# Kernel optimization log

Measured on AMD Instinct MI355X. Metric: run time of the kernel, lower is better.

## Reference

```python
import jax, jax.numpy as jnp
import numpy as np

D_MODEL = 256
NHEAD = 8
NLAYERS = 4
DFF = 1024
PATCH = 8
INPUT = 32
C = 2
DATA_DIM = C * PATCH * PATCH  # 128
P = (INPUT // PATCH) ** 2     # 16
NEG = -1.0e6                  # _neg_large_for_dtype(float32)
EPS = 1e-5


def _ln(x, w, b):
    m = x.mean(-1, keepdims=True)
    v = ((x - m) ** 2).mean(-1, keepdims=True)
    return (x - m) / jnp.sqrt(v + EPS) * w + b


def _forward(img_baseline, acq_dts_float, nan_token, pad_embed, emb_w, emb_b, spatial_pos,
             t_w1, t_b1, t_w2, t_b2, t_w3, t_b3,
             in_proj_w, in_proj_b, out_proj_w, out_proj_b,
             lin1_w, lin1_b, lin2_w, lin2_b, norm1_w, norm1_b, norm2_w, norm2_b,
             mean_w1, mean_b1, mean_w2, mean_b2, lv_w1, lv_b1, lv_w2, lv_b2):
    B, T, Cc, Hh, Ww = img_baseline.shape
    p = PATCH
    gh, gw = Hh // p, Ww // p
    L = T * P
    frame_pad = jnp.all(img_baseline == -9999.0, axis=(2, 3, 4))  # (B,T)
    nan_pix = jnp.isnan(img_baseline)
    token = jnp.clip(nan_token, -10.0, 10.0).reshape(1, 1, Cc, 1, 1)
    x = jnp.clip(jnp.where(nan_pix, token, img_baseline), -10.0, 10.0)

    def patchify(a):  # b t c (h ph)(w pw) -> b t (h w) (c ph pw)
        return a.reshape(B, T, Cc, gh, p, gw, p).transpose(0, 1, 3, 5, 2, 4, 6).reshape(B, T, P, Cc * p * p)

    xp = patchify(x)
    seq_nan = patchify(nan_pix).all(-1).reshape(B, L)
    seq_pad = jnp.broadcast_to(frame_pad[:, :, None], (B, T, P)).reshape(B, L)

    # temporal MLP embedding
    t_in = jnp.where(jnp.isnan(acq_dts_float), 0.0, acq_dts_float)[..., None]  # (B,T,1)
    h = jax.nn.relu(t_in @ t_w1.T + t_b1)
    h = jax.nn.relu(h @ t_w2.T + t_b2)
    temb = h @ t_w3.T + t_b3  # (B,T,D)

    z = xp @ emb_w.T + emb_b + spatial_pos + temb[:, :, None, :]  # (B,T,P,D)
    z = z.reshape(B, L, D_MODEL)
    z = jnp.where(seq_pad[..., None], pad_embed, z)  # masked_scatter of pad_embed

    # additive attention mask: rows with NaN/pad patches are fully masked except diagonal
    masked_rows = seq_nan | seq_pad
    mask = jnp.broadcast_to(jnp.where(masked_rows[:, :, None], NEG, 0.0), (B, L, L))
    eye = jnp.eye(L, dtype=bool)
    mask = jnp.where(eye[None, :, :] & masked_rows[:, :, None], 0.0, mask)
    # key_padding_mask merged additively on key columns
    mask = mask + jnp.where(seq_pad[:, None, :], NEG, 0.0)
    mask = mask[:, None, :, :]  # (B,1,L,L), shared across heads

    dh = D_MODEL // NHEAD
    scale = 1.0 / np.sqrt(dh).astype(np.float32)
    for l in range(NLAYERS):
        qkv = z @ in_proj_w[l].T + in_proj_b[l]
        q, k, v = jnp.split(qkv, 3, axis=-1)
        q = q.reshape(B, L, NHEAD, dh).transpose(0, 2, 1, 3)
        k = k.reshape(B, L, NHEAD, dh).transpose(0, 2, 1, 3)
        v = v.reshape(B, L, NHEAD, dh).transpose(0, 2, 1, 3)
        scores = jnp.einsum('bhqd,bhkd->bhqk', q, k) * scale + mask
        attn = jax.nn.softmax(scores, axis=-1)
        o = jnp.einsum('bhqk,bhkd->bhqd', attn, v).transpose(0, 2, 1, 3).reshape(B, L, D_MODEL)
        o = o @ out_proj_w[l].T + out_proj_b[l]
        z = _ln(z + o, norm1_w[l], norm1_b[l])
        ff = jax.nn.relu(z @ lin1_w[l].T + lin1_b[l]) @ lin2_w[l].T + lin2_b[l]
        z = _ln(z + ff, norm2_w[l], norm2_b[l])

    mean = jnp.clip(jax.nn.relu(z @ mean_w1.T + mean_b1) @ mean_w2.T + mean_b2, -10.0, 10.0)
    logvar = jnp.clip(jax.nn.relu(z @ lv_w1.T + lv_b1) @ lv_w2.T + lv_b2, -10.0, 5.0)

    def unpatch(a):  # b t (h w)(c ph pw) -> b t c (h ph)(w pw)
        return a.reshape(B, T, gh, gw, Cc, p, p).transpose(0, 1, 4, 2, 5, 3, 6).reshape(B, T, Cc, Hh, Ww)

    mean = unpatch(mean.reshape(B, T, P, DATA_DIM))
    logvar = unpatch(logvar.reshape(B, T, P, DATA_DIM))
    return mean[:, -1], logvar[:, -1]


def setup_inputs() -> dict:
    key = jax.random.key(0)
    ks = iter(jax.random.split(key, 48))

    def rn(shape, scale=0.02):
        return jax.random.normal(next(ks), shape, dtype=jnp.float32) * scale

    B, T = 4, 64
    z = lambda s: jnp.zeros(s, jnp.float32)
    return {
        'img_baseline': jax.random.normal(next(ks), (B, T, C, INPUT, INPUT), dtype=jnp.float32),
        'acq_dts_float': jax.random.uniform(next(ks), (B, T), dtype=jnp.float32) * 3000.0,
        'nan_token': rn((C,)),
        'pad_embed': rn((1, 1, D_MODEL)),
        'emb_w': rn((D_MODEL, DATA_DIM)),
        'emb_b': z((D_MODEL,)),
        'spatial_pos': rn((1, 1, P, D_MODEL)),
        't_w1': rn((64, 1)), 't_b1': z((64,)),
        't_w2': rn((128, 64)), 't_b2': z((128,)),
        't_w3': rn((D_MODEL, 128)), 't_b3': z((D_MODEL,)),
        'in_proj_w': rn((NLAYERS, 3 * D_MODEL, D_MODEL)),
        'in_proj_b': z((NLAYERS, 3 * D_MODEL)),
        'out_proj_w': rn((NLAYERS, D_MODEL, D_MODEL)),
        'out_proj_b': z((NLAYERS, D_MODEL)),
        'lin1_w': rn((NLAYERS, DFF, D_MODEL)), 'lin1_b': z((NLAYERS, DFF)),
        'lin2_w': rn((NLAYERS, D_MODEL, DFF)), 'lin2_b': z((NLAYERS, D_MODEL)),
        'norm1_w': jnp.ones((NLAYERS, D_MODEL), jnp.float32), 'norm1_b': z((NLAYERS, D_MODEL)),
        'norm2_w': jnp.ones((NLAYERS, D_MODEL), jnp.float32), 'norm2_b': z((NLAYERS, D_MODEL)),
        'mean_w1': rn((DFF, D_MODEL)), 'mean_b1': z((DFF,)),
        'mean_w2': rn((DATA_DIM, DFF)), 'mean_b2': z((DATA_DIM,)),
        'lv_w1': rn((DFF, D_MODEL)), 'lv_b1': z((DFF,)),
        'lv_w2': rn((DATA_DIM, DFF)), 'lv_b2': z((DATA_DIM,)),
    }


def reference(img_baseline, acq_dts_float, nan_token, pad_embed, emb_w, emb_b, spatial_pos,
              t_w1, t_b1, t_w2, t_b2, t_w3, t_b3,
              in_proj_w, in_proj_b, out_proj_w, out_proj_b,
              lin1_w, lin1_b, lin2_w, lin2_b, norm1_w, norm1_b, norm2_w, norm2_b,
              mean_w1, mean_b1, mean_w2, mean_b2, lv_w1, lv_b1, lv_w2, lv_b2):
    return _forward(img_baseline, acq_dts_float, nan_token, pad_embed, emb_w, emb_b, spatial_pos,
                    t_w1, t_b1, t_w2, t_b2, t_w3, t_b3,
                    in_proj_w, in_proj_b, out_proj_w, out_proj_b,
                    lin1_w, lin1_b, lin2_w, lin2_b, norm1_w, norm1_b, norm2_w, norm2_b,
                    mean_w1, mean_b1, mean_w2, mean_b2, lv_w1, lv_b1, lv_w2, lv_b2)
```

## Files before the change

### kernel.cpp

```cpp
#include <hip/hip_runtime.h>
#include <hip/hip_bf16.h>

#define D_MODEL 256
#define NHEAD 8
#define DH 32
#define NLAYERS 4
#define DFF 1024
#define CC 2
#define DATA_DIM 128
#define PP 16
#define TT 64
#define BB 4
#define LL 1024
#define NEGV -1000000.0f

typedef __bf16 bf16_t;
typedef __bf16 bf16x8 __attribute__((ext_vector_type(8)));
typedef __bf16 bf16x4 __attribute__((ext_vector_type(4)));
typedef float v4f __attribute__((ext_vector_type(4)));

__device__ __forceinline__ bool my_isnan(float v) {
    unsigned u = __float_as_uint(v);
    return (u & 0x7fffffffu) > 0x7f800000u;
}

__device__ __forceinline__ void gld16(bf16_t* l, const bf16_t* g) {
    __builtin_amdgcn_global_load_lds(
        (const __attribute__((address_space(1))) void*)g,
        (__attribute__((address_space(3))) void*)l, 16, 0, 0);
}

__global__ void f2b_all_kernel(const float* __restrict__ s0, bf16_t* __restrict__ d0, int n0,
                               const float* __restrict__ s1, bf16_t* __restrict__ d1, int n1,
                               const float* __restrict__ s2, bf16_t* __restrict__ d2, int n2,
                               const float* __restrict__ s3, bf16_t* __restrict__ d3, int n3,
                               const float* __restrict__ s4, bf16_t* __restrict__ d4, int n4,
                               const float* __restrict__ s5, bf16_t* __restrict__ d5, int n5,
                               const float* __restrict__ s6, bf16_t* __restrict__ d6, int n6,
                               const float* __restrict__ s7, bf16_t* __restrict__ d7, int n7,
                               const float* __restrict__ s8, bf16_t* __restrict__ d8, int n8) {
    int i = (blockIdx.x * 256 + threadIdx.x) * 4;
    const float* s;
    bf16_t* d;
    if (i < n0) { s = s0; d = d0; }
    else if ((i -= n0) < n1) { s = s1; d = d1; }
    else if ((i -= n1) < n2) { s = s2; d = d2; }
    else if ((i -= n2) < n3) { s = s3; d = d3; }
    else if ((i -= n3) < n4) { s = s4; d = d4; }
    else if ((i -= n4) < n5) { s = s5; d = d5; }
    else if ((i -= n5) < n6) { s = s6; d = d6; }
    else if ((i -= n6) < n7) { s = s7; d = d7; }
    else if ((i -= n7) < n8) { s = s8; d = d8; }
    else return;
    float4 v = *(const float4*)(s + i);
    bf16x4 o = {(bf16_t)v.x, (bf16_t)v.y, (bf16_t)v.z, (bf16_t)v.w};
    *(bf16x4*)(d + i) = o;
}

__global__ void prep_frame_kernel(const float* __restrict__ img,
                                  const float* __restrict__ acq,
                                  const float* __restrict__ t_w1, const float* __restrict__ t_b1,
                                  const float* __restrict__ t_w2, const float* __restrict__ t_b2,
                                  const float* __restrict__ t_w3, const float* __restrict__ t_b3,
                                  float* __restrict__ temb, int* __restrict__ framepad) {
    int f = blockIdx.x;
    int tid = threadIdx.x;
    __shared__ float h1[64];
    __shared__ float h2[128];
    __shared__ int sAll;
    if (tid == 0) sAll = 1;
    __syncthreads();
    const float* fr = img + (size_t)f * (CC * 32 * 32);
    bool allpad = true;
    #pragma unroll
    for (int i = 0; i < 8; ++i) {
        float v = fr[tid + i * 256];
        allpad = allpad && (v == -9999.0f);
    }
    if (!allpad) sAll = 0;
    __syncthreads();
    if (tid == 0) framepad[f] = sAll;

    float t_in = acq[f];
    if (my_isnan(t_in)) t_in = 0.0f;
    if (tid < 64) h1[tid] = fmaxf(t_w1[tid] * t_in + t_b1[tid], 0.0f);
    __syncthreads();
    if (tid < 128) {
        float a = t_b2[tid];
        #pragma unroll 8
        for (int j = 0; j < 64; ++j) a += t_w2[tid * 64 + j] * h1[j];
        h2[tid] = fmaxf(a, 0.0f);
    }
    __syncthreads();
    {
        float a = t_b3[tid];
        #pragma unroll 8
        for (int j = 0; j < 128; ++j) a += t_w3[tid * 128 + j] * h2[j];
        temb[(size_t)f * D_MODEL + tid] = a;
    }
}

__global__ __launch_bounds__(256) void patchify_kernel(
    const float* __restrict__ img, const float* __restrict__ nan_token,
    const int* __restrict__ framepad,
    bf16_t* __restrict__ xpb, int* __restrict__ masked_rows,
    float* __restrict__ kmaskf) {
    int tid = threadIdx.x;
    int token = blockIdx.x * 2 + (tid >> 7);
    int dd = tid & 127;
    int l = token & 1023, b = token >> 10;
    int t = l >> 4, p = l & 15;
    int c = dd >> 6, pr = (dd >> 3) & 7, pc = dd & 7;
    int hh = (p >> 2) * 8 + pr, ww = (p & 3) * 8 + pc;
    float v = img[(((size_t)(b * TT + t) * CC + c) * 32 + hh) * 32 + ww];
    bool nanp = my_isnan(v);
    if (nanp) v = fminf(fmaxf(nan_token[c], -10.0f), 10.0f);
    v = fminf(fmaxf(v, -10.0f), 10.0f);
    xpb[(size_t)token * DATA_DIM + dd] = (bf16_t)v;

    __shared__ int wAll[4];
    unsigned long long bal = __ballot(nanp);
    if ((tid & 63) == 0) wAll[tid >> 6] = (bal == 0xFFFFFFFFFFFFFFFFull) ? 1 : 0;
    __syncthreads();
    if (tid < 2) {
        int tk = blockIdx.x * 2 + tid;
        int allnan = wAll[tid * 2] & wAll[tid * 2 + 1];
        int fp = framepad[tk >> 4];
        masked_rows[tk] = allnan | fp;
        kmaskf[tk] = fp ? NEGV : 0.0f;
    }
}

__global__ __launch_bounds__(256) void embed_gemm(
    const bf16_t* __restrict__ X, const bf16_t* __restrict__ W,
    const float* __restrict__ emb_b, const float* __restrict__ spatial,
    const float* __restrict__ temb, const float* __restrict__ pad_embed,
    const int* __restrict__ framepad,
    float* __restrict__ z, bf16_t* __restrict__ zb) {
    __shared__ __align__(16) bf16_t Xs[128 * 32];
    __shared__ __align__(16) bf16_t Ws[64 * 32];
    int tid = threadIdx.x;
    int wave = tid >> 6, lane = tid & 63;
    int quad = lane >> 4, l16 = lane & 15;
    int m0 = blockIdx.y * 128, n0 = blockIdx.x * 64;
    const int K = DATA_DIM, N = D_MODEL;

    v4f acc[2][4];
    #pragma unroll
    for (int i = 0; i < 2; ++i)
        #pragma unroll
        for (int j = 0; j < 4; ++j) acc[i][j] = (v4f){0.f, 0.f, 0.f, 0.f};

    int sr = tid >> 2, ss = tid & 3;
    for (int k0 = 0; k0 < K; k0 += 32) {
        gld16(Xs + tid * 8, X + (size_t)(m0 + sr) * K + k0 + ss * 8);
        gld16(Xs + 2048 + tid * 8, X + (size_t)(m0 + 64 + sr) * K + k0 + ss * 8);
        gld16(Ws + tid * 8, W + (size_t)(n0 + sr) * K + k0 + ss * 8);
        __syncthreads();
        bf16x8 af0 = *(const bf16x8*)(Xs + (wave * 32 + l16) * 32 + quad * 8);
        bf16x8 af1 = *(const bf16x8*)(Xs + (wave * 32 + 16 + l16) * 32 + quad * 8);
        #pragma unroll
        for (int nt = 0; nt < 4; ++nt) {
            bf16x8 bfr = *(const bf16x8*)(Ws + (nt * 16 + l16) * 32 + quad * 8);
            acc[0][nt] = __builtin_amdgcn_mfma_f32_16x16x32_bf16(af0, bfr, acc[0][nt], 0, 0, 0);
            acc[1][nt] = __builtin_amdgcn_mfma_f32_16x16x32_bf16(af1, bfr, acc[1][nt], 0, 0, 0);
        }
        __syncthreads();
    }

    #pragma unroll
    for (int mt = 0; mt < 2; ++mt)
        #pragma unroll
        for (int nt = 0; nt < 4; ++nt) {
            int col = n0 + nt * 16 + l16;
            #pragma unroll
            for (int reg = 0; reg < 4; ++reg) {
                int row = m0 + wave * 32 + mt * 16 + quad * 4 + reg;
                int frame = row >> 4, p = row & 15;
                float v;
                if (framepad[frame]) {
                    v = pad_embed[col];
                } else {
                    v = acc[mt][nt][reg] + emb_b[col] + spatial[p * N + col]
                      + temb[(size_t)frame * N + col];
                }
                z[(size_t)row * N + col] = v;
                zb[(size_t)row * N + col] = (bf16_t)v;
            }
        }
}

template <int MODE, int RELU>
__global__ __launch_bounds__(256) void gemm_mfma(
    const bf16_t* __restrict__ X, const bf16_t* __restrict__ W,
    const float* __restrict__ bias, bf16_t* __restrict__ Y,
    bf16_t* __restrict__ Vt, int M, int N, int K) {
    __shared__ __align__(16) bf16_t Xs[128 * 32];
    __shared__ __align__(16) bf16_t Ws[64 * 32];
    int tid = threadIdx.x;
    int wave = tid >> 6, lane = tid & 63;
    int quad = lane >> 4, l16 = lane & 15;
    int m0 = blockIdx.y * 128, n0 = blockIdx.x * 64;

    v4f acc[2][4];
    #pragma unroll
    for (int i = 0; i < 2; ++i)
        #pragma unroll
        for (int j = 0; j < 4; ++j) acc[i][j] = (v4f){0.f, 0.f, 0.f, 0.f};

    int sr = tid >> 2, ss = tid & 3;
    for (int k0 = 0; k0 < K; k0 += 32) {
        gld16(Xs + tid * 8, X + (size_t)(m0 + sr) * K + k0 + ss * 8);
        gld16(Xs + 2048 + tid * 8, X + (size_t)(m0 + 64 + sr) * K + k0 + ss * 8);
        gld16(Ws + tid * 8, W + (size_t)(n0 + sr) * K + k0 + ss * 8);
        __syncthreads();
        bf16x8 af0 = *(const bf16x8*)(Xs + (wave * 32 + l16) * 32 + quad * 8);
        bf16x8 af1 = *(const bf16x8*)(Xs + (wave * 32 + 16 + l16) * 32 + quad * 8);
        #pragma unroll
        for (int nt = 0; nt < 4; ++nt) {
            bf16x8 bfr = *(const bf16x8*)(Ws + (nt * 16 + l16) * 32 + quad * 8);
            acc[0][nt] = __builtin_amdgcn_mfma_f32_16x16x32_bf16(af0, bfr, acc[0][nt], 0, 0, 0);
            acc[1][nt] = __builtin_amdgcn_mfma_f32_16x16x32_bf16(af1, bfr, acc[1][nt], 0, 0, 0);
        }
        __syncthreads();
    }

    if constexpr (MODE == 1) {
        #pragma unroll
        for (int mt = 0; mt < 2; ++mt)
            #pragma unroll
            for (int nt = 0; nt < 4; ++nt) {
                int col = n0 + nt * 16 + l16;
                float bv = bias[col];
                #pragma unroll
                for (int reg = 0; reg < 4; ++reg) {
                    int row = m0 + wave * 32 + mt * 16 + quad * 4 + reg;
                    float v = acc[mt][nt][reg] + bv;
                    if (RELU) v = fmaxf(v, 0.0f);
                    Y[(size_t)row * N + col] = (bf16_t)v;
                }
            }
    } else {
        if (n0 < 512) {
            #pragma unroll
            for (int mt = 0; mt < 2; ++mt)
                #pragma unroll
                for (int nt = 0; nt < 4; ++nt) {
                    int col = n0 + nt * 16 + l16;
                    float bv = bias[col];
                    #pragma unroll
                    for (int reg = 0; reg < 4; ++reg) {
                        int row = m0 + wave * 32 + mt * 16 + quad * 4 + reg;
                        float v = acc[mt][nt][reg] + bv;
                        Y[(size_t)row * 768 + col] = (bf16_t)v;
                    }
                }
        } else {
            __shared__ __align__(16) bf16_t VT[64 * 136];
            #pragma unroll
            for (int mt = 0; mt < 2; ++mt)
                #pragma unroll
                for (int nt = 0; nt < 4; ++nt) {
                    int cl = nt * 16 + l16;
                    float bv = bias[n0 + cl];
                    #pragma unroll
                    for (int reg = 0; reg < 4; ++reg) {
                        int rl = wave * 32 + mt * 16 + quad * 4 + reg;
                        VT[cl * 136 + rl] = (bf16_t)(acc[mt][nt][reg] + bv);
                    }
                }
            __syncthreads();
            int b = m0 >> 10, l0m = m0 & 1023;
            int cl = tid >> 2;
            int rbase = (tid & 3) * 8;
            int cg = n0 + cl - 512;
            int h = cg >> 5, d = cg & 31;
            bf16_t* dst = Vt + (((size_t)(b * NHEAD + h)) * DH + d) * LL + l0m;
            #pragma unroll
            for (int u = 0; u < 4; ++u)
                *(uint4*)(dst + rbase + u * 32) = *(const uint4*)(VT + cl * 136 + rbase + u * 32);
        }
    }
}

__global__ __launch_bounds__(256) void gemm_small(
    const bf16_t* __restrict__ X, const bf16_t* __restrict__ W,
    const float* __restrict__ bias, const float* __restrict__ Zres,
    float* __restrict__ Y, int M, int N, int K) {
    __shared__ __align__(16) bf16_t Xs[64 * 32];
    __shared__ __align__(16) bf16_t Ws[64 * 32];
    int tid = threadIdx.x;
    int wave = tid >> 6, lane = tid & 63;
    int quad = lane >> 4, l16 = lane & 15;
    int m0 = blockIdx.y * 64, n0 = blockIdx.x * 64;

    v4f acc[4];
    #pragma unroll
    for (int j = 0; j < 4; ++j) acc[j] = (v4f){0.f, 0.f, 0.f, 0.f};

    int sr = tid >> 2, ss = tid & 3;
    for (int k0 = 0; k0 < K; k0 += 32) {
        gld16(Xs + tid * 8, X + (size_t)(m0 + sr) * K + k0 + ss * 8);
        gld16(Ws + tid * 8, W + (size_t)(n0 + sr) * K + k0 + ss * 8);
        __syncthreads();
        bf16x8 af = *(const bf16x8*)(Xs + (wave * 16 + l16) * 32 + quad * 8);
        #pragma unroll
        for (int nt = 0; nt < 4; ++nt) {
            bf16x8 bfr = *(const bf16x8*)(Ws + (nt * 16 + l16) * 32 + quad * 8);
            acc[nt] = __builtin_amdgcn_mfma_f32_16x16x32_bf16(af, bfr, acc[nt], 0, 0, 0);
        }
        __syncthreads();
    }

    #pragma unroll
    for (int nt = 0; nt < 4; ++nt) {
        int col = n0 + nt * 16 + l16;
        float bv = bias[col];
        #pragma unroll
        for (int reg = 0; reg < 4; ++reg) {
            int row = m0 + wave * 16 + quad * 4 + reg;
            Y[(size_t)row * N + col] = acc[nt][reg] + bv + Zres[(size_t)row * N + col];
        }
    }
}

__global__ __launch_bounds__(256) void attn_mfma(
    const bf16_t* __restrict__ qkvb, const bf16_t* __restrict__ Vt,
    const int* __restrict__ masked_rows, const float* __restrict__ kmaskf,
    bf16_t* __restrict__ Ob) {
    __shared__ __align__(16) bf16_t Ks[2][128 * 40];
    __shared__ __align__(16) bf16_t Vs[2][32 * 136];
    __shared__ __align__(16) float  Kms[2][128];
    __shared__ __align__(16) bf16_t Ps[4][16 * 136];

    int tid = threadIdx.x;
    int wave = tid >> 6, lane = tid & 63;
    int quad = lane >> 4, l16 = lane & 15;
    int bid = blockIdx.x;
    int h = bid & 7, b = (bid >> 3) & 3, qt = bid >> 5;
    int q0 = qt * 64 + wave * 16;
    const float scale = 0.17677669529663687f;

    bf16x8 qf = *(const bf16x8*)(qkvb + ((size_t)(b * LL) + q0 + l16) * 768 + h * DH + quad * 8);

    int mq[4];
    #pragma unroll
    for (int reg = 0; reg < 4; ++reg) mq[reg] = masked_rows[b * LL + q0 + quad * 4 + reg];

    float mrun[4], lrun[4];
    v4f oacc[2];
    #pragma unroll
    for (int reg = 0; reg < 4; ++reg) { mrun[reg] = -3.0e38f; lrun[reg] = 0.0f; }
    oacc[0] = (v4f){0.f, 0.f, 0.f, 0.f};
    oacc[1] = (v4f){0.f, 0.f, 0.f, 0.f};

    int kr = tid >> 1, kh = (tid & 1) * 16;
    int vd = tid >> 3, vs0 = (tid & 7) * 8;
    const bf16_t* Kbase = qkvb + (size_t)(b * LL) * 768 + 256 + h * DH;
    const bf16_t* Vbase = Vt + (((size_t)(b * NHEAD + h)) * DH) * LL;
    const float* kmbase = kmaskf + b * LL;

    uint4 ka, kb, va, vb;
    float kmg;
    #define LOADC(c)                                                            \
        do {                                                                    \
            int _k0 = (c) * 128;                                                \
            ka = *(const uint4*)(Kbase + (size_t)(_k0 + kr) * 768 + kh);        \
            kb = *(const uint4*)(Kbase + (size_t)(_k0 + kr) * 768 + kh + 8);    \
            va = *(const uint4*)(Vbase + (size_t)vd * LL + _k0 + vs0);          \
            vb = *(const uint4*)(Vbase + (size_t)vd * LL + _k0 + 64 + vs0);     \
            kmg = (tid < 128) ? kmbase[_k0 + tid] : 0.0f;                       \
        } while (0)
    #define WRITEBUF(buf)                                                       \
        do {                                                                    \
            *(uint4*)(Ks[(buf)] + kr * 40 + kh) = ka;                           \
            *(uint4*)(Ks[(buf)] + kr * 40 + kh + 8) = kb;                       \
            *(uint4*)(Vs[(buf)] + vd * 136 + vs0) = va;                         \
            *(uint4*)(Vs[(buf)] + vd * 136 + 64 + vs0) = vb;                    \
            if (tid < 128) Kms[(buf)][tid] = kmg;                               \
        } while (0)

    LOADC(0);
    WRITEBUF(0);
    LOADC(1);

    bf16_t* Pw = Ps[wave];
    for (int c = 0; c < 8; ++c) {
        __syncthreads();
        int cur = c & 1;
        if (c + 1 < 8) WRITEBUF(cur ^ 1);
        if (c + 2 < 8) LOADC(c + 2);

        int k0 = c * 128;
        const bf16_t* Kc = Ks[cur];
        const bf16_t* Vc = Vs[cur];
        const float* kmc = Kms[cur];

        v4f sf[8];
        #pragma unroll
        for (int nt = 0; nt < 8; ++nt) {
            bf16x8 kf = *(const bf16x8*)(Kc + (nt * 16 + l16) * 40 + quad * 8);
            v4f zf = (v4f){0.f, 0.f, 0.f, 0.f};
            sf[nt] = __builtin_amdgcn_mfma_f32_16x16x32_bf16(qf, kf, zf, 0, 0, 0);
        }

        float sv[8][4];
        #pragma unroll
        for (int nt = 0; nt < 8; ++nt) {
            int kg = k0 + nt * 16 + l16;
            float km = kmc[nt * 16 + l16];
            #pragma unroll
            for (int reg = 0; reg < 4; ++reg) {
                float v = sf[nt][reg] * scale + km;
                if (mq[reg] && (q0 + quad * 4 + reg != kg)) v += NEGV;
                sv[nt][reg] = v;
            }
        }

        float tm[4];
        #pragma unroll
        for (int reg = 0; reg < 4; ++reg) {
            float m = sv[0][reg];
            #pragma unroll
            for (int nt = 1; nt < 8; ++nt) m = fmaxf(m, sv[nt][reg]);
            tm[reg] = m;
        }
        #pragma unroll
        for (int off = 1; off < 16; off <<= 1)
            #pragma unroll
            for (int reg = 0; reg < 4; ++reg) tm[reg] = fmaxf(tm[reg], __shfl_xor(tm[reg], off));

        float alpha[4], psum[4];
        #pragma unroll
        for (int reg = 0; reg < 4; ++reg) {
            float mnew = fmaxf(mrun[reg], tm[reg]);
            alpha[reg] = __expf(mrun[reg] - mnew);
            mrun[reg] = mnew;
            float ps = 0.0f;
            #pragma unroll
            for (int nt = 0; nt < 8; ++nt) {
                float p = __expf(sv[nt][reg] - mnew);
                sv[nt][reg] = p;
                ps += p;
            }
            psum[reg] = ps;
        }
        #pragma unroll
        for (int off = 1; off < 16; off <<= 1)
            #pragma unroll
            for (int reg = 0; reg < 4; ++reg) psum[reg] += __shfl_xor(psum[reg], off);
        #pragma unroll
        for (int reg = 0; reg < 4; ++reg) {
            lrun[reg] = lrun[reg] * alpha[reg] + psum[reg];
            oacc[0][reg] *= alpha[reg];
            oacc[1][reg] *= alpha[reg];
        }

        #pragma unroll
        for (int nt = 0; nt < 8; ++nt)
            #pragma unroll
            for (int reg = 0; reg < 4; ++reg)
                Pw[(quad * 4 + reg) * 136 + nt * 16 + l16] = (bf16_t)sv[nt][reg];

        #pragma unroll
        for (int kt = 0; kt < 4; ++kt) {
            bf16x8 pf = *(const bf16x8*)(Pw + l16 * 136 + kt * 32 + quad * 8);
            #pragma unroll
            for (int nt2 = 0; nt2 < 2; ++nt2) {
                bf16x8 vf = *(const bf16x8*)(Vc + (nt2 * 16 + l16) * 136 + kt * 32 + quad * 8);
                oacc[nt2] = __builtin_amdgcn_mfma_f32_16x16x32_bf16(pf, vf, oacc[nt2], 0, 0, 0);
            }
        }
    }
    #undef LOADC
    #undef WRITEBUF

    #pragma unroll
    for (int nt2 = 0; nt2 < 2; ++nt2)
        #pragma unroll
        for (int reg = 0; reg < 4; ++reg) {
            size_t row = (size_t)(b * LL) + q0 + quad * 4 + reg;
            Ob[row * 256 + h * DH + nt2 * 16 + l16] = (bf16_t)(oacc[nt2][reg] / lrun[reg]);
        }
}

__global__ __launch_bounds__(256) void ln_kernel(
    const float* __restrict__ tmpf, float* __restrict__ z,
    const float* __restrict__ w, const float* __restrict__ b,
    bf16_t* __restrict__ zb) {
    int wave = threadIdx.x >> 6, lane = threadIdx.x & 63;
    int row = blockIdx.x * 4 + wave;
    float4 x = ((const float4*)(tmpf + (size_t)row * D_MODEL))[lane];
    float s = x.x + x.y + x.z + x.w;
    #pragma unroll
    for (int off = 32; off > 0; off >>= 1) s += __shfl_xor(s, off);
    float mean = s * (1.0f / D_MODEL);
    float dx0 = x.x - mean, dx1 = x.y - mean, dx2 = x.z - mean, dx3 = x.w - mean;
    float sq = dx0 * dx0 + dx1 * dx1 + dx2 * dx2 + dx3 * dx3;
    #pragma unroll
    for (int off = 32; off > 0; off >>= 1) sq += __shfl_xor(sq, off);
    float inv = 1.0f / sqrtf(sq * (1.0f / D_MODEL) + 1e-5f);
    float4 wv = ((const float4*)w)[lane];
    float4 bv = ((const float4*)b)[lane];
    float4 r;
    r.x = dx0 * inv * wv.x + bv.x;
    r.y = dx1 * inv * wv.y + bv.y;
    r.z = dx2 * inv * wv.z + bv.z;
    r.w = dx3 * inv * wv.w + bv.w;
    ((float4*)(z + (size_t)row * D_MODEL))[lane] = r;
    bf16x4 rb = {(bf16_t)r.x, (bf16_t)r.y, (bf16_t)r.z, (bf16_t)r.w};
    *(bf16x4*)(zb + (size_t)row * D_MODEL + lane * 4) = rb;
}

__global__ __launch_bounds__(256) void head_h_kernel(
    const bf16_t* __restrict__ zb, const bf16_t* __restrict__ W1b,
    const float* __restrict__ mean_b1, const float* __restrict__ lv_b1,
    bf16_t* __restrict__ hb) {
    __shared__ __align__(16) bf16_t Xs[64 * 32];
    __shared__ __align__(16) bf16_t Ws[64 * 32];
    int tid = threadIdx.x;
    int wave = tid >> 6, lane = tid & 63;
    int quad = lane >> 4, l16 = lane & 15;
    int head = blockIdx.y;
    int n0 = blockIdx.x * 64;
    const bf16_t* W1h = W1b + (size_t)head * DFF * D_MODEL;
    const float* B1f = head ? lv_b1 : mean_b1;
    bf16_t* hbh = hb + (size_t)head * 64 * DFF;

    v4f acc[4];
    #pragma unroll
    for (int j = 0; j < 4; ++j) acc[j] = (v4f){0.f, 0.f, 0.f, 0.f};

    int sr = tid >> 2, ss = tid & 3;
    int gb = sr >> 4, gp = sr & 15;
    const bf16_t* xrow = zb + ((size_t)(gb * LL + (TT - 1) * PP + gp)) * D_MODEL;
    for (int k0 = 0; k0 < D_MODEL; k0 += 32) {
        gld16(Xs + tid * 8, xrow + k0 + ss * 8);
        gld16(Ws + tid * 8, W1h + (size_t)(n0 + sr) * D_MODEL + k0 + ss * 8);
        __syncthreads();
        bf16x8 af = *(const bf16x8*)(Xs + (wave * 16 + l16) * 32 + quad * 8);
        #pragma unroll
        for (int nt = 0; nt < 4; ++nt) {
            bf16x8 bfr = *(const bf16x8*)(Ws + (nt * 16 + l16) * 32 + quad * 8);
            acc[nt] = __builtin_amdgcn_mfma_f32_16x16x32_bf16(af, bfr, acc[nt], 0, 0, 0);
        }
        __syncthreads();
    }

    #pragma unroll
    for (int nt = 0; nt < 4; ++nt) {
        int col = n0 + nt * 16 + l16;
        float bv = B1f[col];
        #pragma unroll
        for (int reg = 0; reg < 4; ++reg) {
            int row = wave * 16 + quad * 4 + reg;
            hbh[(size_t)row * DFF + col] = (bf16_t)fmaxf(acc[nt][reg] + bv, 0.0f);
        }
    }
}

__global__ __launch_bounds__(256) void head_out_kernel(
    const bf16_t* __restrict__ hb, const bf16_t* __restrict__ W2b,
    const float* __restrict__ mean_b2, const float* __restrict__ lv_b2,
    float* __restrict__ out) {
    __shared__ __align__(16) bf16_t hrow[DFF];
    int tid = threadIdx.x;
    int bid = blockIdx.x;
    int head = bid >> 7, rr = (bid >> 1) & 63, half = bid & 1;
    int b = rr >> 4, p = rr & 15;

    if (tid < 128)
        *(uint4*)(hrow + tid * 8) =
            *(const uint4*)(hb + ((size_t)head * 64 + rr) * DFF + tid * 8);
    __syncthreads();

    int ol = tid >> 2, quarter = tid & 3;
    int o = half * 64 + ol;
    const bf16_t* wrow = W2b + ((size_t)head * DATA_DIM + o) * DFF + quarter * 256;
    const bf16_t* hseg = hrow + quarter * 256;
    float acc = 0.0f;
    #pragma unroll 8
    for (int j = 0; j < 32; ++j) {
        bf16x8 w = *(const bf16x8*)(wrow + j * 8);
        bf16x8 hv = *(const bf16x8*)(hseg + j * 8);
        #pragma unroll
        for (int e = 0; e < 8; ++e) acc += (float)w[e] * (float)hv[e];
    }
    acc += __shfl_xor(acc, 1);
    acc += __shfl_xor(acc, 2);
    if (quarter == 0) {
        const float* B2 = head ? lv_b2 : mean_b2;
        float hi = head ? 5.0f : 10.0f;
        float v = fminf(fmaxf(acc + B2[o], -10.0f), hi);
        int c = o >> 6;
        int pr = (o >> 3) & 7, pc = o & 7;
        int hh = (p >> 2) * 8 + pr, ww = (p & 3) * 8 + pc;
        out[(size_t)head * 8192 + ((size_t)(b * CC + c)) * 1024 + hh * 32 + ww] = v;
    }
}

extern "C" void kernel_launch(void* const* d_in, const int* in_sizes, int n_in,
                              void* d_out, int out_size, void* d_ws, size_t ws_size,
                              hipStream_t stream) {
    const float* img        = (const float*)d_in[0];
    const float* acq        = (const float*)d_in[1];
    const float* nan_token  = (const float*)d_in[2];
    const float* pad_embed  = (const float*)d_in[3];
    const float* emb_w      = (const float*)d_in[4];
    const float* emb_b      = (const float*)d_in[5];
    const float* spatial    = (const float*)d_in[6];
    const float* t_w1       = (const float*)d_in[7];
    const float* t_b1       = (const float*)d_in[8];
    const float* t_w2       = (const float*)d_in[9];
    const float* t_b2       = (const float*)d_in[10];
    const float* t_w3       = (const float*)d_in[11];
    const float* t_b3       = (const float*)d_in[12];
    const float* in_proj_w  = (const float*)d_in[13];
    const float* in_proj_b  = (const float*)d_in[14];
    const float* out_proj_w = (const float*)d_in[15];
    const float* out_proj_b = (const float*)d_in[16];
    const float* lin1_w     = (const float*)d_in[17];
    const float* lin1_b     = (const float*)d_in[18];
    const float* lin2_w     = (const float*)d_in[19];
    const float* lin2_b     = (const float*)d_in[20];
    const float* norm1_w    = (const float*)d_in[21];
    const float* norm1_b    = (const float*)d_in[22];
    const float* norm2_w    = (const float*)d_in[23];
    const float* norm2_b    = (const float*)d_in[24];
    const float* mean_w1    = (const float*)d_in[25];
    const float* mean_b1    = (const float*)d_in[26];
    const float* mean_w2    = (const float*)d_in[27];
    const float* mean_b2    = (const float*)d_in[28];
    const float* lv_w1      = (const float*)d_in[29];
    const float* lv_b1      = (const float*)d_in[30];
    const float* lv_w2      = (const float*)d_in[31];
    const float* lv_b2      = (const float*)d_in[32];

    const int M = BB * LL;

    char* wsb = (char*)d_ws;
    float* z       = (float*)wsb;                    wsb += (size_t)M * D_MODEL * 4;
    float* tmpf    = (float*)wsb;                    wsb += (size_t)M * D_MODEL * 4;
    float* temb    = (float*)wsb;                    wsb += (size_t)BB * TT * D_MODEL * 4;
    float* kmaskf  = (float*)wsb;                    wsb += M * 4;
    int* framepad  = (int*)wsb;                      wsb += BB * TT * 4;
    int* masked    = (int*)wsb;                      wsb += M * 4;
    wsb = (char*)(((uintptr_t)wsb + 255) & ~(uintptr_t)255);
    bf16_t* zb     = (bf16_t*)wsb;                   wsb += (size_t)M * D_MODEL * 2;
    bf16_t* xpb    = (bf16_t*)wsb;                   wsb += (size_t)M * DATA_DIM * 2;
    bf16_t* qkvb   = (bf16_t*)wsb;                   wsb += (size_t)M * 768 * 2;
    bf16_t* VtG    = (bf16_t*)wsb;                   wsb += (size_t)M * D_MODEL * 2;
    bf16_t* attnb  = (bf16_t*)wsb;                   wsb += (size_t)M * D_MODEL * 2;
    bf16_t* ff1b   = (bf16_t*)wsb;                   wsb += (size_t)M * DFF * 2;
    bf16_t* inb    = (bf16_t*)wsb;                   wsb += (size_t)NLAYERS * 768 * D_MODEL * 2;
    bf16_t* outb   = (bf16_t*)wsb;                   wsb += (size_t)NLAYERS * D_MODEL * D_MODEL * 2;
    bf16_t* l1b    = (bf16_t*)wsb;                   wsb += (size_t)NLAYERS * DFF * D_MODEL * 2;
    bf16_t* l2b    = (bf16_t*)wsb;                   wsb += (size_t)NLAYERS * D_MODEL * DFF * 2;
    bf16_t* embwb  = (bf16_t*)wsb;                   wsb += (size_t)D_MODEL * DATA_DIM * 2;
    bf16_t* w1b    = (bf16_t*)wsb;                   wsb += (size_t)2 * DFF * D_MODEL * 2;
    bf16_t* w2b    = (bf16_t*)wsb;                   wsb += (size_t)2 * DATA_DIM * DFF * 2;
    bf16_t* hb     = (bf16_t*)wsb;                   wsb += (size_t)2 * 64 * DFF * 2;

    float* outF = (float*)d_out;

    {
        int n1 = NLAYERS * 768 * D_MODEL;
        int n2 = NLAYERS * D_MODEL * D_MODEL;
        int n3 = NLAYERS * DFF * D_MODEL;
        int n4 = NLAYERS * D_MODEL * DFF;
        int n5 = D_MODEL * DATA_DIM;
        int n6 = DFF * D_MODEL;
        int n7 = DFF * D_MODEL;
        int n8 = DATA_DIM * DFF;
        int n9 = DATA_DIM * DFF;
        int tot = n1 + n2 + n3 + n4 + n5 + n6 + n7 + n8 + n9;
        f2b_all_kernel<<<(tot / 4 + 255) / 256, 256, 0, stream>>>(
            in_proj_w, inb, n1, out_proj_w, outb, n2, lin1_w, l1b, n3,
            lin2_w, l2b, n4, emb_w, embwb, n5,
            mean_w1, w1b, n6, lv_w1, w1b + (size_t)DFF * D_MODEL, n7,
            mean_w2, w2b, n8, lv_w2, w2b + (size_t)DATA_DIM * DFF, n9);
    }

    prep_frame_kernel<<<BB * TT, 256, 0, stream>>>(img, acq, t_w1, t_b1, t_w2, t_b2,
                                                   t_w3, t_b3, temb, framepad);
    patchify_kernel<<<M / 2, 256, 0, stream>>>(img, nan_token, framepad, xpb, masked, kmaskf);
    embed_gemm<<<dim3(D_MODEL / 64, M / 128), 256, 0, stream>>>(
        xpb, embwb, emb_b, spatial, temb, pad_embed, framepad, z, zb);

    for (int l = 0; l < NLAYERS; ++l) {
        gemm_mfma<2, 0><<<dim3(768 / 64, M / 128), 256, 0, stream>>>(
            zb, inb + (size_t)l * 768 * D_MODEL, in_proj_b + (size_t)l * 768,
            qkvb, VtG, M, 768, D_MODEL);
        attn_mfma<<<BB * NHEAD * (LL / 64), 256, 0, stream>>>(qkvb, VtG, masked, kmaskf, attnb);
        gemm_small<<<dim3(D_MODEL / 64, M / 64), 256, 0, stream>>>(
            attnb, outb + (size_t)l * D_MODEL * D_MODEL, out_proj_b + (size_t)l * D_MODEL,
            z, tmpf, M, D_MODEL, D_MODEL);
        ln_kernel<<<M / 4, 256, 0, stream>>>(tmpf, z, norm1_w + l * D_MODEL,
                                             norm1_b + l * D_MODEL, zb);
        gemm_mfma<1, 1><<<dim3(DFF / 64, M / 128), 256, 0, stream>>>(
            zb, l1b + (size_t)l * DFF * D_MODEL, lin1_b + (size_t)l * DFF,
            ff1b, nullptr, M, DFF, D_MODEL);
        gemm_small<<<dim3(D_MODEL / 64, M / 64), 256, 0, stream>>>(
            ff1b, l2b + (size_t)l * D_MODEL * DFF, lin2_b + (size_t)l * D_MODEL,
            z, tmpf, M, D_MODEL, DFF);
        ln_kernel<<<M / 4, 256, 0, stream>>>(tmpf, z, norm2_w + l * D_MODEL,
                                             norm2_b + l * D_MODEL, zb);
    }

    head_h_kernel<<<dim3(DFF / 64, 2), 256, 0, stream>>>(zb, w1b, mean_b1, lv_b1, hb);
    head_out_kernel<<<256, 256, 0, stream>>>(hb, w2b, mean_b2, lv_b2, outF);
}
```

Before: 459.8 us.

## Split attention over key halves with merge kernel and shrink GEMM M-tile

Attention is split into two key-range halves (flash-decoding style). Each half writes fp32 partial outputs and running max/sum, and a new merge kernel combines them, doubling the number of attention blocks and shrinking per-block LDS. The QKV and FFN1 GEMMs move from 128-row to 64-row tiles to raise block count on the many-CU GPU. In exchange the change adds an extra kernel launch, fp32 partial traffic, and less per-block data reuse in the GEMMs.

After: 477.8 us. 3.9% more time.

```diff
diff --git a/kernel.cpp b/kernel.cpp
--- a/kernel.cpp
+++ b/kernel.cpp
@@ -191,84 +191,72 @@
 }
 
 template <int MODE, int RELU>
-__global__ __launch_bounds__(256) void gemm_mfma(
+__global__ __launch_bounds__(256) void gemm64(
     const bf16_t* __restrict__ X, const bf16_t* __restrict__ W,
     const float* __restrict__ bias, bf16_t* __restrict__ Y,
     bf16_t* __restrict__ Vt, int M, int N, int K) {
-    __shared__ __align__(16) bf16_t Xs[128 * 32];
+    __shared__ __align__(16) bf16_t Xs[64 * 32];
     __shared__ __align__(16) bf16_t Ws[64 * 32];
     int tid = threadIdx.x;
     int wave = tid >> 6, lane = tid & 63;
     int quad = lane >> 4, l16 = lane & 15;
-    int m0 = blockIdx.y * 128, n0 = blockIdx.x * 64;
-
-    v4f acc[2][4];
-    #pragma unroll
-    for (int i = 0; i < 2; ++i)
-        #pragma unroll
-        for (int j = 0; j < 4; ++j) acc[i][j] = (v4f){0.f, 0.f, 0.f, 0.f};
+    int m0 = blockIdx.y * 64, n0 = blockIdx.x * 64;
+
+    v4f acc[4];
+    #pragma unroll
+    for (int j = 0; j < 4; ++j) acc[j] = (v4f){0.f, 0.f, 0.f, 0.f};
 
     int sr = tid >> 2, ss = tid & 3;
     for (int k0 = 0; k0 < K; k0 += 32) {
         gld16(Xs + tid * 8, X + (size_t)(m0 + sr) * K + k0 + ss * 8);
-        gld16(Xs + 2048 + tid * 8, X + (size_t)(m0 + 64 + sr) * K + k0 + ss * 8);
         gld16(Ws + tid * 8, W + (size_t)(n0 + sr) * K + k0 + ss * 8);
         __syncthreads();
-        bf16x8 af0 = *(const bf16x8*)(Xs + (wave * 32 + l16) * 32 + quad * 8);
-        bf16x8 af1 = *(const bf16x8*)(Xs + (wave * 32 + 16 + l16) * 32 + quad * 8);
+        bf16x8 af = *(const bf16x8*)(Xs + (wave * 16 + l16) * 32 + quad * 8);
         #pragma unroll
         for (int nt = 0; nt < 4; ++nt) {
             bf16x8 bfr = *(const bf16x8*)(Ws + (nt * 16 + l16) * 32 + quad * 8);
-            acc[0][nt] = __builtin_amdgcn_mfma_f32_16x16x32_bf16(af0, bfr, acc[0][nt], 0, 0, 0);
-            acc[1][nt] = __builtin_amdgcn_mfma_f32_16x16x32_bf16(af1, bfr, acc[1][nt], 0, 0, 0);
+            acc[nt] = __builtin_amdgcn_mfma_f32_16x16x32_bf16(af, bfr, acc[nt], 0, 0, 0);
         }
         __syncthreads();
     }
 
     if constexpr (MODE == 1) {
         #pragma unroll
-        for (int mt = 0; mt < 2; ++mt)
+        for (int nt = 0; nt < 4; ++nt) {
+            int col = n0 + nt * 16 + l16;
+            float bv = bias[col];
+            #pragma unroll
+            for (int reg = 0; reg < 4; ++reg) {
+                int row = m0 + wave * 16 + quad * 4 + reg;
+                float v = acc[nt][reg] + bv;
+                if (RELU) v = fmaxf(v, 0.0f);
+                Y[(size_t)row * N + col] = (bf16_t)v;
+            }
+        }
+    } else {
+        if (n0 < 512) {
             #pragma unroll
             for (int nt = 0; nt < 4; ++nt) {
                 int col = n0 + nt * 16 + l16;
                 float bv = bias[col];
                 #pragma unroll
                 for (int reg = 0; reg < 4; ++reg) {
-                    int row = m0 + wave * 32 + mt * 16 + quad * 4 + reg;
-                    float v = acc[mt][nt][reg] + bv;
-                    if (RELU) v = fmaxf(v, 0.0f);
-                    Y[(size_t)row * N + col] = (bf16_t)v;
+                    int row = m0 + wave * 16 + quad * 4 + reg;
+                    Y[(size_t)row * 768 + col] = (bf16_t)(acc[nt][reg] + bv);
                 }
             }
-    } else {
-        if (n0 < 512) {
-            #pragma unroll
-            for (int mt = 0; mt < 2; ++mt)
+        } else {
+            __shared__ __align__(16) bf16_t VT[64 * 72];
+            #pragma unroll
+            for (int nt = 0; nt < 4; ++nt) {
+                int cl = nt * 16 + l16;
+                float bv = bias[n0 + cl];
                 #pragma unroll
-                for (int nt = 0; nt < 4; ++nt) {
-                    int col = n0 + nt * 16 + l16;
-                    float bv = bias[col];
-                    #pragma unroll
-                    for (int reg = 0; reg < 4; ++reg) {
-                        int row = m0 + wave * 32 + mt * 16 + quad * 4 + reg;
-                        float v = acc[mt][nt][reg] + bv;
-                        Y[(size_t)row * 768 + col] = (bf16_t)v;
-                    }
+                for (int reg = 0; reg < 4; ++reg) {
+                    int rl = wave * 16 + quad * 4 + reg;
+                    VT[cl * 72 + rl] = (bf16_t)(acc[nt][reg] + bv);
                 }
-        } else {
-            __shared__ __align__(16) bf16_t VT[64 * 136];
-            #pragma unroll
-            for (int mt = 0; mt < 2; ++mt)
-                #pragma unroll
-                for (int nt = 0; nt < 4; ++nt) {
-                    int cl = nt * 16 + l16;
-                    float bv = bias[n0 + cl];
-                    #pragma unroll
-                    for (int reg = 0; reg < 4; ++reg) {
-                        int rl = wave * 32 + mt * 16 + quad * 4 + reg;
-                        VT[cl * 136 + rl] = (bf16_t)(acc[mt][nt][reg] + bv);
-                    }
-                }
+            }
             __syncthreads();
             int b = m0 >> 10, l0m = m0 & 1023;
             int cl = tid >> 2;
@@ -277,8 +265,8 @@
             int h = cg >> 5, d = cg & 31;
             bf16_t* dst = Vt + (((size_t)(b * NHEAD + h)) * DH + d) * LL + l0m;
             #pragma unroll
-            for (int u = 0; u < 4; ++u)
-                *(uint4*)(dst + rbase + u * 32) = *(const uint4*)(VT + cl * 136 + rbase + u * 32);
+            for (int u = 0; u < 2; ++u)
+                *(uint4*)(dst + rbase + u * 32) = *(const uint4*)(VT + cl * 72 + rbase + u * 32);
         }
     }
 }
@@ -327,18 +315,21 @@
 __global__ __launch_bounds__(256) void attn_mfma(
     const bf16_t* __restrict__ qkvb, const bf16_t* __restrict__ Vt,
     const int* __restrict__ masked_rows, const float* __restrict__ kmaskf,
-    bf16_t* __restrict__ Ob) {
-    __shared__ __align__(16) bf16_t Ks[2][128 * 40];
-    __shared__ __align__(16) bf16_t Vs[2][32 * 136];
-    __shared__ __align__(16) float  Kms[2][128];
-    __shared__ __align__(16) bf16_t Ps[4][16 * 136];
+    float* __restrict__ Opart, float2* __restrict__ mlpart) {
+    __shared__ __align__(16) bf16_t Ks[2][64 * 40];
+    __shared__ __align__(16) bf16_t Vs[2][32 * 72];
+    __shared__ __align__(16) float  Kms[2][64];
+    __shared__ __align__(16) bf16_t Ps[4][16 * 72];
 
     int tid = threadIdx.x;
     int wave = tid >> 6, lane = tid & 63;
     int quad = lane >> 4, l16 = lane & 15;
     int bid = blockIdx.x;
-    int h = bid & 7, b = (bid >> 3) & 3, qt = bid >> 5;
+    int h = bid & 7, b = (bid >> 3) & 3;
+    int r = bid >> 5;
+    int qt = r & 15, s = r >> 4;
     int q0 = qt * 64 + wave * 16;
+    int kbase0 = s * 512;
     const float scale = 0.17677669529663687f;
 
     bf16x8 qf = *(const bf16x8*)(qkvb + ((size_t)(b * LL) + q0 + l16) * 768 + h * DH + quad * 8);
@@ -354,30 +345,26 @@
     oacc[0] = (v4f){0.f, 0.f, 0.f, 0.f};
     oacc[1] = (v4f){0.f, 0.f, 0.f, 0.f};
 
-    int kr = tid >> 1, kh = (tid & 1) * 16;
+    int kr = tid >> 2, ks = (tid & 3) * 8;
     int vd = tid >> 3, vs0 = (tid & 7) * 8;
     const bf16_t* Kbase = qkvb + (size_t)(b * LL) * 768 + 256 + h * DH;
     const bf16_t* Vbase = Vt + (((size_t)(b * NHEAD + h)) * DH) * LL;
     const float* kmbase = kmaskf + b * LL;
 
-    uint4 ka, kb, va, vb;
+    uint4 ka, va;
     float kmg;
     #define LOADC(c)                                                            \
         do {                                                                    \
-            int _k0 = (c) * 128;                                                \
-            ka = *(const uint4*)(Kbase + (size_t)(_k0 + kr) * 768 + kh);        \
-            kb = *(const uint4*)(Kbase + (size_t)(_k0 + kr) * 768 + kh + 8);    \
+            int _k0 = kbase0 + (c) * 64;                                        \
+            ka = *(const uint4*)(Kbase + (size_t)(_k0 + kr) * 768 + ks);        \
             va = *(const uint4*)(Vbase + (size_t)vd * LL + _k0 + vs0);          \
-            vb = *(const uint4*)(Vbase + (size_t)vd * LL + _k0 + 64 + vs0);     \
-            kmg = (tid < 128) ? kmbase[_k0 + tid] : 0.0f;                       \
+            kmg = (tid < 64) ? kmbase[_k0 + tid] : 0.0f;                        \
         } while (0)
     #define WRITEBUF(buf)                                                       \
         do {                                                                    \
-            *(uint4*)(Ks[(buf)] + kr * 40 + kh) = ka;                           \
-            *(uint4*)(Ks[(buf)] + kr * 40 + kh + 8) = kb;                       \
-            *(uint4*)(Vs[(buf)] + vd * 136 + vs0) = va;                         \
-            *(uint4*)(Vs[(buf)] + vd * 136 + 64 + vs0) = vb;                    \
-            if (tid < 128) Kms[(buf)][tid] = kmg;                               \
+            *(uint4*)(Ks[(buf)] + kr * 40 + ks) = ka;                           \
+            *(uint4*)(Vs[(buf)] + vd * 72 + vs0) = va;                          \
+            if (tid < 64) Kms[(buf)][tid] = kmg;                                \
         } while (0)
 
     LOADC(0);
@@ -391,22 +378,22 @@
         if (c + 1 < 8) WRITEBUF(cur ^ 1);
         if (c + 2 < 8) LOADC(c + 2);
 
-        int k0 = c * 128;
+        int k0 = kbase0 + c * 64;
         const bf16_t* Kc = Ks[cur];
         const bf16_t* Vc = Vs[cur];
         const float* kmc = Kms[cur];
 
-        v4f sf[8];
-        #pragma unroll
-        for (int nt = 0; nt < 8; ++nt) {
+        v4f sf[4];
+        #pragma unroll
+        for (int nt = 0; nt < 4; ++nt) {
             bf16x8 kf = *(const bf16x8*)(Kc + (nt * 16 + l16) * 40 + quad * 8);
             v4f zf = (v4f){0.f, 0.f, 0.f, 0.f};
             sf[nt] = __builtin_amdgcn_mfma_f32_16x16x32_bf16(qf, kf, zf, 0, 0, 0);
         }
 
-        float sv[8][4];
-        #pragma unroll
-        for (int nt = 0; nt < 8; ++nt) {
+        float sv[4][4];
+        #pragma unroll
+        for (int nt = 0; nt < 4; ++nt) {
             int kg = k0 + nt * 16 + l16;
             float km = kmc[nt * 16 + l16];
             #pragma unroll
@@ -421,8 +408,7 @@
         #pragma unroll
         for (int reg = 0; reg < 4; ++reg) {
             float m = sv[0][reg];
-            #pragma unroll
-            for (int nt = 1; nt < 8; ++nt) m = fmaxf(m, sv[nt][reg]);
+            m = fmaxf(m, sv[1][reg]); m = fmaxf(m, sv[2][reg]); m = fmaxf(m, sv[3][reg]);
             tm[reg] = m;
         }
         #pragma unroll
@@ -438,7 +424,7 @@
             mrun[reg] = mnew;
             float ps = 0.0f;
             #pragma unroll
-            for (int nt = 0; nt < 8; ++nt) {
+            for (int nt = 0; nt < 4; ++nt) {
                 float p = __expf(sv[nt][reg] - mnew);
                 sv[nt][reg] = p;
                 ps += p;
@@ -457,17 +443,17 @@
         }
 
         #pragma unroll
-        for (int nt = 0; nt < 8; ++nt)
+        for (int nt = 0; nt < 4; ++nt)
             #pragma unroll
             for (int reg = 0; reg < 4; ++reg)
-                Pw[(quad * 4 + reg) * 136 + nt * 16 + l16] = (bf16_t)sv[nt][reg];
-
-        #pragma unroll
-        for (int kt = 0; kt < 4; ++kt) {
-            bf16x8 pf = *(const bf16x8*)(Pw + l16 * 136 + kt * 32 + quad * 8);
+                Pw[(quad * 4 + reg) * 72 + nt * 16 + l16] = (bf16_t)sv[nt][reg];
+
+        #pragma unroll
+        for (int kt = 0; kt < 2; ++kt) {
+            bf16x8 pf = *(const bf16x8*)(Pw + l16 * 72 + kt * 32 + quad * 8);
             #pragma unroll
             for (int nt2 = 0; nt2 < 2; ++nt2) {
-                bf16x8 vf = *(const bf16x8*)(Vc + (nt2 * 16 + l16) * 136 + kt * 32 + quad * 8);
+                bf16x8 vf = *(const bf16x8*)(Vc + (nt2 * 16 + l16) * 72 + kt * 32 + quad * 8);
                 oacc[nt2] = __builtin_amdgcn_mfma_f32_16x16x32_bf16(pf, vf, oacc[nt2], 0, 0, 0);
             }
         }
@@ -476,12 +462,30 @@
     #undef WRITEBUF
 
     #pragma unroll
-    for (int nt2 = 0; nt2 < 2; ++nt2)
-        #pragma unroll
-        for (int reg = 0; reg < 4; ++reg) {
-            size_t row = (size_t)(b * LL) + q0 + quad * 4 + reg;
-            Ob[row * 256 + h * DH + nt2 * 16 + l16] = (bf16_t)(oacc[nt2][reg] / lrun[reg]);
-        }
+    for (int reg = 0; reg < 4; ++reg) {
+        size_t grow = (size_t)s * (BB * LL) + b * LL + q0 + quad * 4 + reg;
+        #pragma unroll
+        for (int nt2 = 0; nt2 < 2; ++nt2)
+            Opart[grow * 256 + h * DH + nt2 * 16 + l16] = oacc[nt2][reg];
+        if (l16 == 0)
+            mlpart[grow * NHEAD + h] = make_float2(mrun[reg], lrun[reg]);
+    }
+}
+
+__global__ __launch_bounds__(256) void attn_merge(
+    const float* __restrict__ Opart, const float2* __restrict__ mlpart,
+    bf16_t* __restrict__ attnb) {
+    int row = blockIdx.x;
+    int col = threadIdx.x;
+    int h = col >> 5;
+    float2 ml1 = mlpart[(size_t)row * NHEAD + h];
+    float2 ml2 = mlpart[((size_t)(BB * LL) + row) * NHEAD + h];
+    float mm = fmaxf(ml1.x, ml2.x);
+    float e1 = __expf(ml1.x - mm), e2 = __expf(ml2.x - mm);
+    float denom = e1 * ml1.y + e2 * ml2.y;
+    float o1 = Opart[(size_t)row * 256 + col];
+    float o2 = Opart[((size_t)(BB * LL) + row) * 256 + col];
+    attnb[(size_t)row * 256 + col] = (bf16_t)((e1 * o1 + e2 * o2) / denom);
 }
 
 __global__ __launch_bounds__(256) void ln_kernel(
@@ -641,8 +645,10 @@
     char* wsb = (char*)d_ws;
     float* z       = (float*)wsb;                    wsb += (size_t)M * D_MODEL * 4;
     float* tmpf    = (float*)wsb;                    wsb += (size_t)M * D_MODEL * 4;
+    float* Opart   = (float*)wsb;                    wsb += (size_t)2 * M * D_MODEL * 4;
     float* temb    = (float*)wsb;                    wsb += (size_t)BB * TT * D_MODEL * 4;
     float* kmaskf  = (float*)wsb;                    wsb += M * 4;
+    float2* mlpart = (float2*)wsb;                   wsb += (size_t)2 * M * NHEAD * 8;
     int* framepad  = (int*)wsb;                      wsb += BB * TT * 4;
     int* masked    = (int*)wsb;                      wsb += M * 4;
     wsb = (char*)(((uintptr_t)wsb + 255) & ~(uintptr_t)255);
@@ -688,16 +694,18 @@
         xpb, embwb, emb_b, spatial, temb, pad_embed, framepad, z, zb);
 
     for (int l = 0; l < NLAYERS; ++l) {
-        gemm_mfma<2, 0><<<dim3(768 / 64, M / 128), 256, 0, stream>>>(
+        gemm64<2, 0><<<dim3(768 / 64, M / 64), 256, 0, stream>>>(
             zb, inb + (size_t)l * 768 * D_MODEL, in_proj_b + (size_t)l * 768,
             qkvb, VtG, M, 768, D_MODEL);
-        attn_mfma<<<BB * NHEAD * (LL / 64), 256, 0, stream>>>(qkvb, VtG, masked, kmaskf, attnb);
+        attn_mfma<<<2 * BB * NHEAD * (LL / 64), 256, 0, stream>>>(
+            qkvb, VtG, masked, kmaskf, Opart, mlpart);
+        attn_merge<<<M, 256, 0, stream>>>(Opart, mlpart, attnb);
         gemm_small<<<dim3(D_MODEL / 64, M / 64), 256, 0, stream>>>(
             attnb, outb + (size_t)l * D_MODEL * D_MODEL, out_proj_b + (size_t)l * D_MODEL,
             z, tmpf, M, D_MODEL, D_MODEL);
         ln_kernel<<<M / 4, 256, 0, stream>>>(tmpf, z, norm1_w + l * D_MODEL,
                                              norm1_b + l * D_MODEL, zb);
-        gemm_mfma<1, 1><<<dim3(DFF / 64, M / 128), 256, 0, stream>>>(
+        gemm64<1, 1><<<dim3(DFF / 64, M / 64), 256, 0, stream>>>(
             zb, l1b + (size_t)l * DFF * D_MODEL, lin1_b + (size_t)l * DFF,
             ff1b, nullptr, M, DFF, D_MODEL);
         gemm_small<<<dim3(D_MODEL / 64, M / 64), 256, 0, stream>>>(
```
